# Kernel optimization log

Measured on AMD Instinct MI355X. Metric: run time of the kernel, lower is better.

Reference implementation:

```python
import jax, jax.numpy as jnp
import numpy as np

P_BINS = 5
T_BINS = 16
B_BINS = P_BINS * T_BINS  # 80
IN_CH = 16
OUT_CH = 32
N_VERTS = 30000   # mesh vertices (cols of conn)
N_PATCH = 30000   # patches (rows of conn / B)
K_NNZ = 3         # nnz per sparse row (interpolation support)


def setup_inputs() -> dict:
    key = jax.random.key(0)
    k1, k2, k3, k4 = jax.random.split(key, 4)
    x = jax.random.normal(k1, (N_VERTS, IN_CH), dtype=jnp.float32)
    conn_idx = jax.random.randint(k2, (N_PATCH * B_BINS, K_NNZ), 0, N_VERTS, dtype=jnp.int32)
    conn_val = jax.random.uniform(k3, (N_PATCH * B_BINS, K_NNZ), dtype=jnp.float32)
    weights = jax.random.normal(k4, (B_BINS, IN_CH, OUT_CH), dtype=jnp.float32)
    return {"x": x, "conn_idx": conn_idx, "conn_val": conn_val, "weights": weights}


def _rotated_weights(weights):
    # layer_weights[j, :, :, i] = weights[(j + p*i) % B]  -> reshape (B*inp, out*t)
    j = jnp.arange(B_BINS)[:, None]
    i = jnp.arange(T_BINS)[None, :]
    idx = (j + P_BINS * i) % B_BINS                       # (B, t)
    lw = weights[idx]                                     # (B, t, inp, out)
    lw = jnp.transpose(lw, (0, 2, 3, 1))                  # (B, inp, out, t)
    return lw.reshape(B_BINS * IN_CH, OUT_CH * T_BINS)


def reference(x, conn_idx, conn_val, weights):
    # sparse.mm(conn, x): gather K vertex features per bin row and weight-sum
    gathered = jnp.einsum('rk,rkc->rc', conn_val, x[conn_idx])  # (N*B, inp)
    h = gathered.reshape(-1, B_BINS * IN_CH)                    # (N, B*inp)
    lw = _rotated_weights(weights)                              # (B*inp, out*t)
    y = h @ lw                                                  # (N, out*t)
    y = y.reshape(-1, OUT_CH, T_BINS)
    return jnp.max(y, axis=-1)                                  # (N, out)
```

## Files before the change

kernel.cpp:

```cpp
#include <hip/hip_runtime.h>
#include <hip/hip_bf16.h>
#include <stdint.h>

#define NP 30000
#define BBINS 80
#define INCH 16
#define OUTCH 32
#define KDIM 1280
#define NDIM 512
#define KSTEPS 40
#define MTILES 235

typedef __bf16 bf16x8 __attribute__((ext_vector_type(8)));
typedef float f32x4 __attribute__((ext_vector_type(4)));

__device__ __forceinline__ void async_ld16(const void* g, void* l) {
    __builtin_amdgcn_global_load_lds(
        (const __attribute__((address_space(1))) unsigned int*)g,
        (__attribute__((address_space(3))) unsigned int*)l,
        16, 0, 0);
}

__global__ void prep_wc(const float* __restrict__ w, __bf16* __restrict__ wc) {
    int gid = blockIdx.x * 256 + threadIdx.x;
    int c   = gid & 15;
    int o   = (gid >> 4) & 31;
    int bid = gid >> 9;
    wc[gid] = (__bf16)w[(bid * INCH + c) * OUTCH + o];
}

__global__ __launch_bounds__(512, 1) void fused_gemm_max(
    const float* __restrict__ x,
    const int*   __restrict__ cidx,
    const float* __restrict__ cval,
    const __bf16* __restrict__ wc,
    float* __restrict__ out) {

    __shared__ __align__(16) __bf16 Wlds[80 * 32 * 16];
    __shared__ __align__(16) __bf16 Alds[128 * 32];

    const int tid  = threadIdx.x;
    const int lane = tid & 63;
    const int wave = tid >> 6;
    const int wave_mrow = wave >> 2;
    const int wave_ncol = wave & 3;
    const int mbase = blockIdx.x * 128;

    {
        const char* src = (const char*)wc;
        char* dst = (char*)Wlds + tid * 16;
#pragma unroll
        for (int i = 0; i < 10; ++i) {
            const int byte = tid * 16 + i * 8192;
            const int bid  = byte >> 10;
            async_ld16(src + (byte ^ ((bid & 7) << 4)), dst + i * 8192);
        }
    }

    const int patch_l = tid >> 2;
    const int chunk   = tid & 3;
    const int bin_l   = chunk >> 1;
    const int half    = chunk & 1;
    int p = mbase + patch_l;
    if (p > NP - 1) p = NP - 1;
    const int row0 = p * BBINS + bin_l;
    char* aW = (char*)Alds + patch_l * 64
             + ((chunk ^ ((patch_l >> 1) & 3)) << 4);

    const int ml = lane & 15, q = lane >> 4;
    const int f  = (ml >> 1) & 3;
    int a_off[4];
#pragma unroll
    for (int i = 0; i < 4; ++i)
        a_off[i] = (wave_mrow * 64 + i * 16 + ml) * 64 + ((q ^ f) << 4);
    const int ch = q & 1;
    int vj4[8];
#pragma unroll
    for (int j = 0; j < 8; ++j) {
        const int o = wave_ncol * 8 + j;
        vj4[j] = (o * 2 + ch) << 4;
    }
    int bid = (q >> 1) + 5 * ml;

    f32x4 acc[4][8];
#pragma unroll
    for (int i = 0; i < 4; ++i)
#pragma unroll
        for (int j = 0; j < 8; ++j)
            acc[i][j] = (f32x4){0.f, 0.f, 0.f, 0.f};

    int r3 = row0 * 3;
    float va0 = cval[r3], va1 = cval[r3 + 1], va2 = cval[r3 + 2];
    int   ia0 = cidx[r3], ia1 = cidx[r3 + 1], ia2 = cidx[r3 + 2];
    const float* xp;
    xp = x + (size_t)(unsigned)ia0 * 16 + half * 8;
    float4 xa0 = *(const float4*)xp, xa1 = *(const float4*)(xp + 4);
    xp = x + (size_t)(unsigned)ia1 * 16 + half * 8;
    float4 xa2 = *(const float4*)xp, xa3 = *(const float4*)(xp + 4);
    xp = x + (size_t)(unsigned)ia2 * 16 + half * 8;
    float4 xa4 = *(const float4*)xp, xa5 = *(const float4*)(xp + 4);
    r3 = (row0 + 2) * 3;
    int   ib0 = cidx[r3], ib1 = cidx[r3 + 1], ib2 = cidx[r3 + 2];
    float vb0 = cval[r3], vb1 = cval[r3 + 1], vb2 = cval[r3 + 2];

    for (int kc = 0; kc < KSTEPS; ++kc) {
        bf16x8 hv;
        hv[0] = (__bf16)(va0 * xa0.x + va1 * xa2.x + va2 * xa4.x);
        hv[1] = (__bf16)(va0 * xa0.y + va1 * xa2.y + va2 * xa4.y);
        hv[2] = (__bf16)(va0 * xa0.z + va1 * xa2.z + va2 * xa4.z);
        hv[3] = (__bf16)(va0 * xa0.w + va1 * xa2.w + va2 * xa4.w);
        hv[4] = (__bf16)(va0 * xa1.x + va1 * xa3.x + va2 * xa5.x);
        hv[5] = (__bf16)(va0 * xa1.y + va1 * xa3.y + va2 * xa5.y);
        hv[6] = (__bf16)(va0 * xa1.z + va1 * xa3.z + va2 * xa5.z);
        hv[7] = (__bf16)(va0 * xa1.w + va1 * xa3.w + va2 * xa5.w);
        *(bf16x8*)aW = hv;

        float4 nx0 = xa0, nx1 = xa1, nx2 = xa2, nx3 = xa3, nx4 = xa4, nx5 = xa5;
        if (kc + 1 < KSTEPS) {
            xp = x + (size_t)(unsigned)ib0 * 16 + half * 8;
            nx0 = *(const float4*)xp; nx1 = *(const float4*)(xp + 4);
            xp = x + (size_t)(unsigned)ib1 * 16 + half * 8;
            nx2 = *(const float4*)xp; nx3 = *(const float4*)(xp + 4);
            xp = x + (size_t)(unsigned)ib2 * 16 + half * 8;
            nx4 = *(const float4*)xp; nx5 = *(const float4*)(xp + 4);
        }
        int   ni0 = ib0, ni1 = ib1, ni2 = ib2;
        float nv0 = vb0, nv1 = vb1, nv2 = vb2;
        if (kc + 2 < KSTEPS) {
            r3 = (row0 + (kc + 2) * 2) * 3;
            ni0 = cidx[r3 + 0]; ni1 = cidx[r3 + 1]; ni2 = cidx[r3 + 2];
            nv0 = cval[r3 + 0]; nv1 = cval[r3 + 1]; nv2 = cval[r3 + 2];
        }

        asm volatile("s_waitcnt lgkmcnt(0)" ::: "memory");
        __builtin_amdgcn_s_barrier();
        __builtin_amdgcn_sched_barrier(0);

        bf16x8 af[4], bfr[8];
#pragma unroll
        for (int i = 0; i < 4; ++i)
            af[i] = *(const bf16x8*)((const char*)Alds + a_off[i]);
        const int bidK = bid << 10;
        const int b74  = (bid & 7) << 4;
#pragma unroll
        for (int j = 0; j < 8; ++j)
            bfr[j] = *(const bf16x8*)((const char*)Wlds + (bidK + (vj4[j] ^ b74)));
#pragma unroll
        for (int i = 0; i < 4; ++i)
#pragma unroll
            for (int j = 0; j < 8; ++j)
                acc[i][j] = __builtin_amdgcn_mfma_f32_16x16x32_bf16(
                    af[i], bfr[j], acc[i][j], 0, 0, 0);

        asm volatile("s_waitcnt lgkmcnt(0)" ::: "memory");
        __builtin_amdgcn_s_barrier();
        __builtin_amdgcn_sched_barrier(0);

        va0 = vb0; va1 = vb1; va2 = vb2;
        xa0 = nx0; xa1 = nx1; xa2 = nx2; xa3 = nx3; xa4 = nx4; xa5 = nx5;
        ib0 = ni0; ib1 = ni1; ib2 = ni2;
        vb0 = nv0; vb1 = nv1; vb2 = nv2;
        bid += 2;
        if (bid >= BBINS) bid -= BBINS;
    }

    const int rgrp = lane >> 4;
    const int tl   = lane & 15;
#pragma unroll
    for (int i = 0; i < 4; ++i) {
#pragma unroll
        for (int j = 0; j < 8; ++j) {
            float v0 = acc[i][j][0], v1 = acc[i][j][1];
            float v2 = acc[i][j][2], v3 = acc[i][j][3];
#pragma unroll
            for (int off = 1; off < 16; off <<= 1) {
                v0 = fmaxf(v0, __shfl_xor(v0, off));
                v1 = fmaxf(v1, __shfl_xor(v1, off));
                v2 = fmaxf(v2, __shfl_xor(v2, off));
                v3 = fmaxf(v3, __shfl_xor(v3, off));
            }
            if (tl == 0) {
                const int o  = wave_ncol * 8 + j;
                const int pr = mbase + wave_mrow * 64 + i * 16 + rgrp * 4;
                if (pr + 0 < NP) out[(pr + 0) * 32 + o] = v0;
                if (pr + 1 < NP) out[(pr + 1) * 32 + o] = v1;
                if (pr + 2 < NP) out[(pr + 2) * 32 + o] = v2;
                if (pr + 3 < NP) out[(pr + 3) * 32 + o] = v3;
            }
        }
    }
}

extern "C" void kernel_launch(void* const* d_in, const int* in_sizes, int n_in,
                              void* d_out, int out_size, void* d_ws, size_t ws_size,
                              hipStream_t stream) {
    const float* x    = (const float*)d_in[0];
    const int*   cidx = (const int*)d_in[1];
    const float* cval = (const float*)d_in[2];
    const float* w    = (const float*)d_in[3];
    float* out = (float*)d_out;

    __bf16* wc = (__bf16*)d_ws;

    hipLaunchKernelGGL(prep_wc, dim3(160), dim3(256), 0, stream, w, wc);
    hipLaunchKernelGGL(fused_gemm_max, dim3(MTILES), dim3(512), 0, stream,
                       x, cidx, cval, (const __bf16*)wc, out);
}
```

Measured before the change: 168.7 us.

## Double K-chunk per iteration to halve barriers, each thread gathering full rows

Each loop iteration now handles two K sub-steps (64 K values) instead of one, which halves the iteration count and the number of block barriers. The A tile in LDS doubles to 128x64 with an 8-way XOR swizzle. Each thread now gathers and combines a full 16-channel bin row instead of half a row. The cost is more registers for the prefetched x values and a larger LDS footprint.

```diff
diff --git a/kernel.cpp b/kernel.cpp
--- a/kernel.cpp
+++ b/kernel.cpp
@@ -8,7 +8,7 @@
 #define OUTCH 32
 #define KDIM 1280
 #define NDIM 512
-#define KSTEPS 40
+#define KSTEPS 20
 #define MTILES 235
 
 typedef __bf16 bf16x8 __attribute__((ext_vector_type(8)));
@@ -37,7 +37,7 @@
     float* __restrict__ out) {
 
     __shared__ __align__(16) __bf16 Wlds[80 * 32 * 16];
-    __shared__ __align__(16) __bf16 Alds[128 * 32];
+    __shared__ __align__(16) __bf16 Alds[128 * 64];
 
     const int tid  = threadIdx.x;
     const int lane = tid & 63;
@@ -58,21 +58,22 @@
     }
 
     const int patch_l = tid >> 2;
-    const int chunk   = tid & 3;
-    const int bin_l   = chunk >> 1;
-    const int half    = chunk & 1;
+    const int tq      = tid & 3;
     int p = mbase + patch_l;
     if (p > NP - 1) p = NP - 1;
-    const int row0 = p * BBINS + bin_l;
-    char* aW = (char*)Alds + patch_l * 64
-             + ((chunk ^ ((patch_l >> 1) & 3)) << 4);
+    const int row0 = p * BBINS + tq;
+    const int pswz = (patch_l & 7);
+    char* aW0 = (char*)Alds + patch_l * 128 + (((2 * tq + 0) ^ pswz) << 4);
+    char* aW1 = (char*)Alds + patch_l * 128 + (((2 * tq + 1) ^ pswz) << 4);
 
     const int ml = lane & 15, q = lane >> 4;
-    const int f  = (ml >> 1) & 3;
-    int a_off[4];
-#pragma unroll
-    for (int i = 0; i < 4; ++i)
-        a_off[i] = (wave_mrow * 64 + i * 16 + ml) * 64 + ((q ^ f) << 4);
+    int a_off[2][4];
+#pragma unroll
+    for (int ks = 0; ks < 2; ++ks)
+#pragma unroll
+        for (int i = 0; i < 4; ++i)
+            a_off[ks][i] = (wave_mrow * 64 + i * 16 + ml) * 128
+                         + (((ks * 4 + q) ^ (ml & 7)) << 4);
     const int ch = q & 1;
     int vj4[8];
 #pragma unroll
@@ -80,7 +81,7 @@
         const int o = wave_ncol * 8 + j;
         vj4[j] = (o * 2 + ch) << 4;
     }
-    int bid = (q >> 1) + 5 * ml;
+    int bid0 = (q >> 1) + 5 * ml;
 
     f32x4 acc[4][8];
 #pragma unroll
@@ -90,44 +91,53 @@
             acc[i][j] = (f32x4){0.f, 0.f, 0.f, 0.f};
 
     int r3 = row0 * 3;
+    int   ia0 = cidx[r3], ia1 = cidx[r3 + 1], ia2 = cidx[r3 + 2];
     float va0 = cval[r3], va1 = cval[r3 + 1], va2 = cval[r3 + 2];
-    int   ia0 = cidx[r3], ia1 = cidx[r3 + 1], ia2 = cidx[r3 + 2];
-    const float* xp;
-    xp = x + (size_t)(unsigned)ia0 * 16 + half * 8;
-    float4 xa0 = *(const float4*)xp, xa1 = *(const float4*)(xp + 4);
-    xp = x + (size_t)(unsigned)ia1 * 16 + half * 8;
-    float4 xa2 = *(const float4*)xp, xa3 = *(const float4*)(xp + 4);
-    xp = x + (size_t)(unsigned)ia2 * 16 + half * 8;
-    float4 xa4 = *(const float4*)xp, xa5 = *(const float4*)(xp + 4);
-    r3 = (row0 + 2) * 3;
+    f32x4 xa[3][4];
+    {
+        const f32x4* xp0 = (const f32x4*)(x + (size_t)(unsigned)ia0 * 16);
+        const f32x4* xp1 = (const f32x4*)(x + (size_t)(unsigned)ia1 * 16);
+        const f32x4* xp2 = (const f32x4*)(x + (size_t)(unsigned)ia2 * 16);
+#pragma unroll
+        for (int u = 0; u < 4; ++u) {
+            xa[0][u] = xp0[u]; xa[1][u] = xp1[u]; xa[2][u] = xp2[u];
+        }
+    }
+    r3 = (row0 + 4) * 3;
     int   ib0 = cidx[r3], ib1 = cidx[r3 + 1], ib2 = cidx[r3 + 2];
     float vb0 = cval[r3], vb1 = cval[r3 + 1], vb2 = cval[r3 + 2];
 
     for (int kc = 0; kc < KSTEPS; ++kc) {
-        bf16x8 hv;
-        hv[0] = (__bf16)(va0 * xa0.x + va1 * xa2.x + va2 * xa4.x);
-        hv[1] = (__bf16)(va0 * xa0.y + va1 * xa2.y + va2 * xa4.y);
-        hv[2] = (__bf16)(va0 * xa0.z + va1 * xa2.z + va2 * xa4.z);
-        hv[3] = (__bf16)(va0 * xa0.w + va1 * xa2.w + va2 * xa4.w);
-        hv[4] = (__bf16)(va0 * xa1.x + va1 * xa3.x + va2 * xa5.x);
-        hv[5] = (__bf16)(va0 * xa1.y + va1 * xa3.y + va2 * xa5.y);
-        hv[6] = (__bf16)(va0 * xa1.z + va1 * xa3.z + va2 * xa5.z);
-        hv[7] = (__bf16)(va0 * xa1.w + va1 * xa3.w + va2 * xa5.w);
-        *(bf16x8*)aW = hv;
-
-        float4 nx0 = xa0, nx1 = xa1, nx2 = xa2, nx3 = xa3, nx4 = xa4, nx5 = xa5;
+        bf16x8 hv0, hv1;
+#pragma unroll
+        for (int e = 0; e < 4; ++e) {
+            hv0[e]     = (__bf16)(va0 * xa[0][0][e] + va1 * xa[1][0][e] + va2 * xa[2][0][e]);
+            hv0[e + 4] = (__bf16)(va0 * xa[0][1][e] + va1 * xa[1][1][e] + va2 * xa[2][1][e]);
+            hv1[e]     = (__bf16)(va0 * xa[0][2][e] + va1 * xa[1][2][e] + va2 * xa[2][2][e]);
+            hv1[e + 4] = (__bf16)(va0 * xa[0][3][e] + va1 * xa[1][3][e] + va2 * xa[2][3][e]);
+        }
+        *(bf16x8*)aW0 = hv0;
+        *(bf16x8*)aW1 = hv1;
+
+        f32x4 nx[3][4];
+#pragma unroll
+        for (int v = 0; v < 3; ++v)
+#pragma unroll
+            for (int u = 0; u < 4; ++u)
+                nx[v][u] = xa[v][u];
         if (kc + 1 < KSTEPS) {
-            xp = x + (size_t)(unsigned)ib0 * 16 + half * 8;
-            nx0 = *(const float4*)xp; nx1 = *(const float4*)(xp + 4);
-            xp = x + (size_t)(unsigned)ib1 * 16 + half * 8;
-            nx2 = *(const float4*)xp; nx3 = *(const float4*)(xp + 4);
-            xp = x + (size_t)(unsigned)ib2 * 16 + half * 8;
-            nx4 = *(const float4*)xp; nx5 = *(const float4*)(xp + 4);
+            const f32x4* xp0 = (const f32x4*)(x + (size_t)(unsigned)ib0 * 16);
+            const f32x4* xp1 = (const f32x4*)(x + (size_t)(unsigned)ib1 * 16);
+            const f32x4* xp2 = (const f32x4*)(x + (size_t)(unsigned)ib2 * 16);
+#pragma unroll
+            for (int u = 0; u < 4; ++u) {
+                nx[0][u] = xp0[u]; nx[1][u] = xp1[u]; nx[2][u] = xp2[u];
+            }
         }
         int   ni0 = ib0, ni1 = ib1, ni2 = ib2;
         float nv0 = vb0, nv1 = vb1, nv2 = vb2;
         if (kc + 2 < KSTEPS) {
-            r3 = (row0 + (kc + 2) * 2) * 3;
+            r3 = (row0 + (kc + 2) * 4) * 3;
             ni0 = cidx[r3 + 0]; ni1 = cidx[r3 + 1]; ni2 = cidx[r3 + 2];
             nv0 = cval[r3 + 0]; nv1 = cval[r3 + 1]; nv2 = cval[r3 + 2];
         }
@@ -136,32 +146,41 @@
         __builtin_amdgcn_s_barrier();
         __builtin_amdgcn_sched_barrier(0);
 
-        bf16x8 af[4], bfr[8];
-#pragma unroll
-        for (int i = 0; i < 4; ++i)
-            af[i] = *(const bf16x8*)((const char*)Alds + a_off[i]);
-        const int bidK = bid << 10;
-        const int b74  = (bid & 7) << 4;
-#pragma unroll
-        for (int j = 0; j < 8; ++j)
-            bfr[j] = *(const bf16x8*)((const char*)Wlds + (bidK + (vj4[j] ^ b74)));
-#pragma unroll
-        for (int i = 0; i < 4; ++i)
+#pragma unroll
+        for (int ks = 0; ks < 2; ++ks) {
+            int bid = bid0 + 2 * ks;
+            if (bid >= BBINS) bid -= BBINS;
+            const int bidK = bid << 10;
+            const int b74  = (bid & 7) << 4;
+            bf16x8 af[4], bfr[8];
+#pragma unroll
+            for (int i = 0; i < 4; ++i)
+                af[i] = *(const bf16x8*)((const char*)Alds + a_off[ks][i]);
 #pragma unroll
             for (int j = 0; j < 8; ++j)
-                acc[i][j] = __builtin_amdgcn_mfma_f32_16x16x32_bf16(
-                    af[i], bfr[j], acc[i][j], 0, 0, 0);
+                bfr[j] = *(const bf16x8*)((const char*)Wlds + (bidK + (vj4[j] ^ b74)));
+#pragma unroll
+            for (int i = 0; i < 4; ++i)
+#pragma unroll
+                for (int j = 0; j < 8; ++j)
+                    acc[i][j] = __builtin_amdgcn_mfma_f32_16x16x32_bf16(
+                        af[i], bfr[j], acc[i][j], 0, 0, 0);
+        }
 
         asm volatile("s_waitcnt lgkmcnt(0)" ::: "memory");
         __builtin_amdgcn_s_barrier();
         __builtin_amdgcn_sched_barrier(0);
 
         va0 = vb0; va1 = vb1; va2 = vb2;
-        xa0 = nx0; xa1 = nx1; xa2 = nx2; xa3 = nx3; xa4 = nx4; xa5 = nx5;
+#pragma unroll
+        for (int v = 0; v < 3; ++v)
+#pragma unroll
+            for (int u = 0; u < 4; ++u)
+                xa[v][u] = nx[v][u];
         ib0 = ni0; ib1 = ni1; ib2 = ni2;
         vb0 = nv0; vb1 = nv1; vb2 = nv2;
-        bid += 2;
-        if (bid >= BBINS) bid -= BBINS;
+        bid0 += 4;
+        if (bid0 >= BBINS) bid0 -= BBINS;
     }
 
     const int rgrp = lane >> 4;
```

Result: slower. 175.1 us (+3.8%).
